# Kernel tuning notes

Measured on AMD Instinct MI355X. Metric: run time of the kernel, lower is better.

Reference implementation:

```python
import jax, jax.numpy as jnp
import numpy as np

B, S, D, H = 8, 1024, 512, 8
HD = D // H
EPS = 1e-5


def layer_norm(x, g, b):
    m = jnp.mean(x, axis=-1, keepdims=True)
    v = jnp.mean(jnp.square(x - m), axis=-1, keepdims=True)
    return (x - m) * jax.lax.rsqrt(v + EPS) * g + b


def mha(x, w_in, b_in, w_out, b_out):
    # x: [B,S,D]; w_in: [3D,D]; PyTorch MultiheadAttention math (no dropout, eval)
    b, s, d = x.shape
    qkv = x @ w_in.T + b_in                      # [B,S,3D]
    q, k, v = jnp.split(qkv, 3, axis=-1)
    q = q.reshape(b, s, H, HD)
    k = k.reshape(b, s, H, HD)
    v = v.reshape(b, s, H, HD)
    scores = jnp.einsum('bqhd,bkhd->bhqk', q, k) / np.sqrt(HD)
    a = jax.nn.softmax(scores, axis=-1)
    o = jnp.einsum('bhqk,bkhd->bqhd', a, v).reshape(b, s, d)
    return o @ w_out.T + b_out


def interp_linear(y, out_size):
    # y: [B,S_in,D]; torch F.interpolate(mode='linear', align_corners=False)
    s_in = y.shape[1]
    scale = s_in / out_size
    src = (jnp.arange(out_size, dtype=jnp.float32) + 0.5) * scale - 0.5
    src = jnp.clip(src, 0.0, s_in - 1.0)
    i0 = jnp.floor(src).astype(jnp.int32)
    i1 = jnp.minimum(i0 + 1, s_in - 1)
    w = (src - i0.astype(jnp.float32))[None, :, None]
    return y[:, i0, :] * (1.0 - w) + y[:, i1, :] * w


def setup_inputs() -> dict:
    key = jax.random.key(0)
    ks = jax.random.split(key, 16)
    sd = 0.02
    return {
        'x': jax.random.normal(ks[0], (B, S, D), jnp.float32),
        'w_in1': jax.random.normal(ks[1], (3 * D, D), jnp.float32) * sd,
        'b_in1': jnp.zeros((3 * D,), jnp.float32),
        'w_out1': jax.random.normal(ks[2], (D, D), jnp.float32) * sd,
        'b_out1': jnp.zeros((D,), jnp.float32),
        'w_in2': jax.random.normal(ks[3], (3 * D, D), jnp.float32) * sd,
        'b_in2': jnp.zeros((3 * D,), jnp.float32),
        'w_out2': jax.random.normal(ks[4], (D, D), jnp.float32) * sd,
        'b_out2': jnp.zeros((D,), jnp.float32),
        'g1': jnp.ones((D,), jnp.float32), 'beta1': jnp.zeros((D,), jnp.float32),
        'g2': jnp.ones((D,), jnp.float32), 'beta2': jnp.zeros((D,), jnp.float32),
        'g3': jnp.ones((D,), jnp.float32), 'beta3': jnp.zeros((D,), jnp.float32),
        'w_ff1': jax.random.normal(ks[5], (4 * D, D), jnp.float32) * sd,
        'b_ff1': jnp.zeros((4 * D,), jnp.float32),
        'w_ff2': jax.random.normal(ks[6], (D, 4 * D), jnp.float32) * sd,
        'b_ff2': jnp.zeros((D,), jnp.float32),
    }


def reference(x, w_in1, b_in1, w_out1, b_out1, w_in2, b_in2, w_out2, b_out2,
              g1, beta1, g2, beta2, g3, beta3, w_ff1, b_ff1, w_ff2, b_ff2):
    a1 = mha(x, w_in1, b_in1, w_out1, b_out1)
    x = layer_norm(x + a1, g1, beta1)
    # avg_pool1d kernel=2 stride=2 ceil_mode (S even -> exact halving)
    pooled = x.reshape(B, S // 2, 2, D).mean(axis=2)
    a2 = mha(pooled, w_in2, b_in2, w_out2, b_out2)
    up = interp_linear(a2, S)
    x = layer_norm(x + up, g2, beta2)
    h = jax.nn.gelu(x @ w_ff1.T + b_ff1, approximate=False)
    ff = h @ w_ff2.T + b_ff2
    return layer_norm(x + ff, g3, beta3)
```

## Files before the change

kernel.cpp:

```cpp
#include <hip/hip_runtime.h>
#include <hip/hip_bf16.h>
#include <math.h>

typedef __hip_bfloat16 bf16;
typedef __attribute__((ext_vector_type(8))) short short8;
typedef __attribute__((ext_vector_type(4))) float f32x4;
typedef __attribute__((ext_vector_type(16))) float f32x16;

__device__ __forceinline__ float ldf(const float* p, size_t i) { return p[i]; }
__device__ __forceinline__ float ldf(const bf16*  p, size_t i) { return __bfloat162float(p[i]); }
__device__ __forceinline__ void  stf(float* p, size_t i, float v) { p[i] = v; }
__device__ __forceinline__ void  stf(bf16*  p, size_t i, float v) { p[i] = __float2bfloat16(v); }

__device__ __forceinline__ float ex2(float x) { return __builtin_amdgcn_exp2f(x); }

__device__ __forceinline__ void gl16(const void* gp, void* lp) {
    __builtin_amdgcn_global_load_lds(
        (const __attribute__((address_space(1))) void*)gp,
        (__attribute__((address_space(3))) void*)lp, 16, 0, 0);
}

__device__ __forceinline__ void pl32swap(unsigned &a, unsigned &b) {
    asm volatile("v_permlane32_swap_b32 %0, %1" : "+v"(a), "+v"(b));
}

__global__ __launch_bounds__(256) void cvt_kernel(
    const float* __restrict__ src, bf16* __restrict__ dst, int n)
{
    for (int i = blockIdx.x * 256 + threadIdx.x; i < n; i += gridDim.x * 256)
        dst[i] = __float2bfloat16(src[i]);
}

__global__ __launch_bounds__(256) void cvt_w(
    const float* __restrict__ s0, const float* __restrict__ s1,
    const float* __restrict__ s2, const float* __restrict__ s3,
    const float* __restrict__ s4, const float* __restrict__ s5,
    bf16* __restrict__ dst)
{
    int i = blockIdx.x * 256 + threadIdx.x;
    const float* s; int off;
    if      (i <  786432) { s = s0; off = 0; }
    else if (i < 1048576) { s = s1; off =  786432; }
    else if (i < 1835008) { s = s2; off = 1048576; }
    else if (i < 2097152) { s = s3; off = 1835008; }
    else if (i < 3145728) { s = s4; off = 2097152; }
    else                  { s = s5; off = 3145728; }
    dst[i] = __float2bfloat16(s[i - off]);
}

__global__ __launch_bounds__(256) void vtrans(
    const bf16* __restrict__ qkv, bf16* __restrict__ vt, int S)
{
    __shared__ bf16 t[64][72];
    const int tid = threadIdx.x;
    const int s0 = blockIdx.x * 64;
    const int bh = blockIdx.y;
    const int b = bh >> 3, h = bh & 7;
    const int rr = tid >> 3, c8 = (tid & 7) * 8;
    #pragma unroll
    for (int p = 0; p < 2; p++) {
        int row = p * 32 + rr;
        *(short8*)&t[row][c8] =
            *(const short8*)&qkv[(size_t)(b * S + s0 + row) * 1536 + 1024 + h * 64 + c8];
    }
    __syncthreads();
    #pragma unroll
    for (int p = 0; p < 2; p++) {
        int d = p * 32 + rr;
        union { bf16 v[8]; short8 s; } pk;
        #pragma unroll
        for (int j = 0; j < 8; j++) pk.v[j] = t[c8 + j][d];
        *(short8*)&vt[(size_t)(bh * 64 + d) * S + s0 + c8] = pk.s;
    }
}

template <int EPI>
__global__ __launch_bounds__(256) void gemm_rs(
    const bf16* __restrict__ A, const bf16* __restrict__ W,
    const float* __restrict__ bias, bf16* __restrict__ C,
    int M, int N, int K)
{
    __shared__ __align__(16) bf16 Asl[2][128 * 64];
    __shared__ __align__(16) bf16 Bsl[2][128 * 64];

    const int tid  = threadIdx.x;
    const int lane = tid & 63;
    const int wave = tid >> 6;
    const int wm   = wave >> 1, wn = wave & 1;
    const int l15  = lane & 15, quad = lane >> 4;

    const int nwg = gridDim.x * gridDim.y;
    const int bid = blockIdx.y * gridDim.x + blockIdx.x;
    const int wid = (bid & 7) * (nwg >> 3) + (bid >> 3);
    const int bx  = wid % gridDim.x, by = wid / gridDim.x;
    const int row0 = by * 128, col0 = bx * 128;

    const int sr = tid >> 3;
    const int gg = tid & 7;

    const bf16* As[4]; const bf16* Ws[4]; int lo[4];
    #pragma unroll
    for (int j = 0; j < 4; j++) {
        int row = j * 32 + sr;
        int gs  = (gg ^ (row & 7)) * 8;
        As[j] = &A[(size_t)(row0 + row) * K + gs];
        Ws[j] = &W[(size_t)(col0 + row) * K + gs];
        lo[j] = row * 64 + gg * 8;
    }

    short8 ga[4], gb[4];
    auto LOADG = [&](int k0) {
        #pragma unroll
        for (int j = 0; j < 4; j++) ga[j] = *(const short8*)(As[j] + k0);
        #pragma unroll
        for (int j = 0; j < 4; j++) gb[j] = *(const short8*)(Ws[j] + k0);
    };
    auto WRITEL = [&](int buf) {
        #pragma unroll
        for (int j = 0; j < 4; j++) {
            *(short8*)&Asl[buf][lo[j]] = ga[j];
            *(short8*)&Bsl[buf][lo[j]] = gb[j];
        }
    };

    f32x4 acc[4][4] = {};
    const int nk = K >> 6;

    LOADG(0);
    WRITEL(0);
    __syncthreads();

    int cur = 0;
    for (int i = 0; i < nk; i++) {
        if (i + 1 < nk) LOADG((i + 1) << 6);

        #pragma unroll
        for (int ks = 0; ks < 64; ks += 32) {
            short8 af[4], bfr[4];
            const int g0 = (ks >> 3) + quad;
            const int col = (g0 ^ (l15 & 7)) * 8;
            #pragma unroll
            for (int mt = 0; mt < 4; mt++)
                af[mt] = *(const short8*)&Asl[cur][(wm * 64 + mt * 16 + l15) * 64 + col];
            #pragma unroll
            for (int nt = 0; nt < 4; nt++)
                bfr[nt] = *(const short8*)&Bsl[cur][(wn * 64 + nt * 16 + l15) * 64 + col];
            #pragma unroll
            for (int mt = 0; mt < 4; mt++)
                #pragma unroll
                for (int nt = 0; nt < 4; nt++)
                    acc[mt][nt] = __builtin_amdgcn_mfma_f32_16x16x32_bf16(
                        af[mt], bfr[nt], acc[mt][nt], 0, 0, 0);
        }

        if (i + 1 < nk) WRITEL(cur ^ 1);
        __syncthreads();
        cur ^= 1;
    }

    #pragma unroll
    for (int mt = 0; mt < 4; mt++) {
        int row = row0 + wm * 64 + mt * 16 + quad * 4;
        #pragma unroll
        for (int nt = 0; nt < 4; nt++) {
            int col = col0 + wn * 64 + nt * 16 + l15;
            float bv = bias[col];
            #pragma unroll
            for (int r = 0; r < 4; r++) {
                float v = acc[mt][nt][r] + bv;
                if (EPI == 1) v = 0.5f * v * (1.0f + erff(v * 0.70710678118654752f));
                C[(size_t)(row + r) * N + col] = __float2bfloat16(v);
            }
        }
    }
}

template <int LQB>
__global__ __launch_bounds__(128) void flash_attn_mfma(
    const bf16* __restrict__ qkv, const bf16* __restrict__ vt,
    bf16* __restrict__ o)
{
    constexpr int S  = 64 << LQB;
    constexpr int nt = 1 << LQB;

    __shared__ __align__(16) bf16 Kl[2][64 * 64];

    const int tid  = threadIdx.x;
    const int wave = tid >> 6, lane = tid & 63;
    const int l31  = lane & 31, hi = lane >> 5;

    const int r    = blockIdx.x;
    const int w    = (r & 7) * ((1 << LQB) * 8) + (r >> 3);
    const int qblk = w & ((1 << LQB) - 1);
    const int bh   = w >> LQB;
    const int h    = bh & 7, bb = bh >> 3;
    const int q0   = qblk * 64 + wave * 32;

    const bf16* base  = qkv + (size_t)bb * S * 1536 + h * 64;
    const bf16* vbase = vt + (size_t)bh * 64 * S;

    short8 qf[4];
    #pragma unroll
    for (int c = 0; c < 4; c++)
        qf[c] = *(const short8*)&base[(size_t)(q0 + l31) * 1536 + c * 16 + hi * 8];

    const int sr = lane >> 3;
    const int sc = ((lane & 7) ^ sr) * 8;

    auto STGK = [&](int buf, int k0) {
        #pragma unroll
        for (int t = 0; t < 4; t++) {
            int r0 = wave * 32 + t * 8;
            gl16(&base[(size_t)(k0 + r0 + sr) * 1536 + 512 + sc], &Kl[buf][r0 * 64]);
        }
    };

    f32x16 oacc[2] = {};
    float lrow = 0.f;
    const float CE = 0.18033688f;

    STGK(0, 0);

    for (int it = 0; it < nt; it++) {
        const int cur = it & 1;
        __syncthreads();
        if (it + 1 < nt) STGK(cur ^ 1, (it + 1) << 6);

        short8 vf[2][2][2];
        {
            const bf16* vb = vbase + (it << 6) + hi * 8;
            #pragma unroll
            for (int dt = 0; dt < 2; dt++) {
                const bf16* vd = &vb[(size_t)(dt * 32 + l31) * S];
                #pragma unroll
                for (int sub = 0; sub < 2; sub++)
                    #pragma unroll
                    for (int kk = 0; kk < 2; kk++)
                        vf[sub][kk][dt] = *(const short8*)&vd[sub * 32 + kk * 16];
            }
        }

        const bf16* Kc = &Kl[cur][0];
        #pragma unroll
        for (int sub = 0; sub < 2; sub++) {
            f32x16 st = {};
            #pragma unroll
            for (int c = 0; c < 4; c++) {
                const int row  = sub * 32 + l31;
                const int slot = (c * 2 + hi) ^ (row & 7);
                short8 af = *(const short8*)&Kc[row * 64 + slot * 8];
                st = __builtin_amdgcn_mfma_f32_32x32x16_bf16(af, qf[c], st, 0, 0, 0);
            }

            float p[16]; float ps = 0.f;
            #pragma unroll
            for (int r2 = 0; r2 < 16; r2++) {
                p[r2] = ex2(st[r2] * CE - 2.0f);
                ps += p[r2];
            }
            lrow += ps;

            unsigned wk[8];
            #pragma unroll
            for (int j = 0; j < 8; j++)
                asm("v_cvt_pk_bf16_f32 %0, %1, %2" : "=v"(wk[j]) : "v"(p[2*j]), "v"(p[2*j+1]));

            #pragma unroll
            for (int kk = 0; kk < 2; kk++) {
                pl32swap(wk[kk*4+0], wk[kk*4+2]);
                pl32swap(wk[kk*4+1], wk[kk*4+3]);
                union { unsigned u[4]; short8 s; } pa;
                pa.u[0] = wk[kk*4+0]; pa.u[1] = wk[kk*4+1];
                pa.u[2] = wk[kk*4+2]; pa.u[3] = wk[kk*4+3];
                #pragma unroll
                for (int dt = 0; dt < 2; dt++)
                    oacc[dt] = __builtin_amdgcn_mfma_f32_32x32x16_bf16(
                        pa.s, vf[sub][kk][dt], oacc[dt], 0, 0, 0);
            }
        }
    }

    lrow += __shfl_xor(lrow, 32);
    float inv = 1.0f / lrow;
    #pragma unroll
    for (int r2 = 0; r2 < 16; r2++) {
        int qr = (r2 & 3) + 8 * (r2 >> 2) + 4 * hi;
        float iv = __shfl(inv, qr);
        size_t rb = ((size_t)bb * S + q0 + qr) * 512 + h * 64;
        o[rb + l31]      = __float2bfloat16(oacc[0][r2] * iv);
        o[rb + 32 + l31] = __float2bfloat16(oacc[1][r2] * iv);
    }
}

template <typename AT, typename OT, bool INTERP>
__global__ __launch_bounds__(256) void ln_kernel(
    const AT* __restrict__ a, const bf16* __restrict__ bsrc,
    const float* __restrict__ g, const float* __restrict__ beta,
    OT* __restrict__ out)
{
    const int row = blockIdx.x;
    const int t = threadIdx.x;
    const size_t base = (size_t)row * 512;

    float a0 = ldf(a, base + t), a1 = ldf(a, base + t + 256);
    float b0, b1;
    if (INTERP) {
        int s = row & 1023, bb = row >> 10;
        float src = fminf(fmaxf((s + 0.5f) * 0.5f - 0.5f, 0.f), 511.f);
        int i0 = (int)src;
        int i1 = min(i0 + 1, 511);
        float w = src - (float)i0;
        size_t r0 = ((size_t)bb * 512 + i0) * 512;
        size_t r1 = ((size_t)bb * 512 + i1) * 512;
        b0 = __bfloat162float(bsrc[r0 + t]) * (1.f - w) + __bfloat162float(bsrc[r1 + t]) * w;
        b1 = __bfloat162float(bsrc[r0 + t + 256]) * (1.f - w) + __bfloat162float(bsrc[r1 + t + 256]) * w;
    } else {
        b0 = __bfloat162float(bsrc[base + t]);
        b1 = __bfloat162float(bsrc[base + t + 256]);
    }
    float v0 = a0 + b0, v1 = a1 + b1;

    __shared__ float red[4];
    const int lane = t & 63, wid = t >> 6;

    float sm = v0 + v1;
    #pragma unroll
    for (int off = 32; off > 0; off >>= 1) sm += __shfl_xor(sm, off);
    if (lane == 0) red[wid] = sm;
    __syncthreads();
    sm = red[0] + red[1] + red[2] + red[3];
    const float mean = sm * (1.0f / 512.0f);

    float d0 = v0 - mean, d1 = v1 - mean;
    float vv = d0 * d0 + d1 * d1;
    __syncthreads();
    #pragma unroll
    for (int off = 32; off > 0; off >>= 1) vv += __shfl_xor(vv, off);
    if (lane == 0) red[wid] = vv;
    __syncthreads();
    vv = red[0] + red[1] + red[2] + red[3];
    const float rstd = rsqrtf(vv * (1.0f / 512.0f) + 1e-5f);

    stf(out, base + t,       d0 * rstd * g[t]       + beta[t]);
    stf(out, base + t + 256, d1 * rstd * g[t + 256] + beta[t + 256]);
}

__global__ __launch_bounds__(256) void pool_kernel(
    const bf16* __restrict__ x, bf16* __restrict__ p)
{
    size_t i = (size_t)blockIdx.x * 256 + threadIdx.x;
    size_t d = i & 511;
    size_t rs = i >> 9;
    size_t b = rs >> 9, s = rs & 511;
    size_t r = (b * 1024 + 2 * s) * 512 + d;
    p[i] = __float2bfloat16(0.5f * (__bfloat162float(x[r]) + __bfloat162float(x[r + 512])));
}

extern "C" void kernel_launch(void* const* d_in, const int* in_sizes, int n_in,
                              void* d_out, int out_size, void* d_ws, size_t ws_size,
                              hipStream_t stream)
{
    const float* x      = (const float*)d_in[0];
    const float* w_in1  = (const float*)d_in[1];
    const float* b_in1  = (const float*)d_in[2];
    const float* w_out1 = (const float*)d_in[3];
    const float* b_out1 = (const float*)d_in[4];
    const float* w_in2  = (const float*)d_in[5];
    const float* b_in2  = (const float*)d_in[6];
    const float* w_out2 = (const float*)d_in[7];
    const float* b_out2 = (const float*)d_in[8];
    const float* g1     = (const float*)d_in[9];
    const float* be1    = (const float*)d_in[10];
    const float* g2     = (const float*)d_in[11];
    const float* be2    = (const float*)d_in[12];
    const float* g3     = (const float*)d_in[13];
    const float* be3    = (const float*)d_in[14];
    const float* w_ff1  = (const float*)d_in[15];
    const float* b_ff1  = (const float*)d_in[16];
    const float* w_ff2  = (const float*)d_in[17];
    const float* b_ff2  = (const float*)d_in[18];

    bf16* ws     = (bf16*)d_ws;
    bf16* xb     = ws + 0;
    bf16* wq1    = ws + 4194304;
    bf16* wo1    = ws + 4980736;
    bf16* wq2    = ws + 5242880;
    bf16* wo2    = ws + 6029312;
    bf16* wf1    = ws + 6291456;
    bf16* wf2    = ws + 7340032;
    bf16* qkv1   = ws + 8388608;
    bf16* o1     = ws + 20971520;
    bf16* a1     = ws + 25165824;
    bf16* x1     = ws + 29360128;
    bf16* pooled = ws + 33554432;
    bf16* qkv2   = ws + 35651584;
    bf16* o2     = ws + 41943040;
    bf16* a2     = ws + 44040192;
    bf16* x2     = ws + 46137344;
    bf16* h      = ws + 8388608;
    bf16* ff     = ws + 25165824;
    bf16* vt     = ws + 46137344;

    dim3 blk(256);
    dim3 fblk(128);

    cvt_kernel<<<4096, blk, 0, stream>>>(x, xb, 4194304);
    cvt_w<<<16384, blk, 0, stream>>>(w_in1, w_out1, w_in2, w_out2, w_ff1, w_ff2, wq1);

    gemm_rs<0><<<dim3(12, 64), blk, 0, stream>>>(xb, wq1, b_in1, qkv1, 8192, 1536, 512);
    vtrans<<<dim3(16, 64), blk, 0, stream>>>(qkv1, vt, 1024);
    flash_attn_mfma<4><<<dim3(1024), fblk, 0, stream>>>(qkv1, vt, o1);
    gemm_rs<0><<<dim3(4, 64), blk, 0, stream>>>(o1, wo1, b_out1, a1, 8192, 512, 512);
    ln_kernel<float, bf16, false><<<8192, blk, 0, stream>>>(x, a1, g1, be1, x1);
    pool_kernel<<<8192, blk, 0, stream>>>(x1, pooled);
    gemm_rs<0><<<dim3(12, 32), blk, 0, stream>>>(pooled, wq2, b_in2, qkv2, 4096, 1536, 512);
    vtrans<<<dim3(8, 64), blk, 0, stream>>>(qkv2, vt, 512);
    flash_attn_mfma<3><<<dim3(512), fblk, 0, stream>>>(qkv2, vt, o2);
    gemm_rs<0><<<dim3(4, 32), blk, 0, stream>>>(o2, wo2, b_out2, a2, 4096, 512, 512);
    ln_kernel<bf16, bf16, true><<<8192, blk, 0, stream>>>(x1, a2, g2, be2, x2);
    gemm_rs<1><<<dim3(16, 64), blk, 0, stream>>>(x2, wf1, b_ff1, h, 8192, 2048, 512);
    gemm_rs<0><<<dim3(4, 64), blk, 0, stream>>>(h, wf2, b_ff2, ff, 8192, 512, 2048);
    ln_kernel<bf16, float, false><<<8192, blk, 0, stream>>>(x2, ff, g3, be3, (float*)d_out);
}
```

Baseline: 322.4 us.

## Fuse V transpose into QKV GEMM epilogue, fuse LN with pooling, narrow N tiles

The QKV projection GEMM now writes the V columns straight into the transposed vt layout in its epilogue, so the separate vtrans kernels go away. The first layernorm and the average pool are merged into one kernel that handles row pairs and writes both x1 and pooled. The GEMM gains a BN template parameter, and the N=512 GEMMs and the second QKV GEMM use 64-wide tiles to launch more workgroups. Together these cut kernel launches and the extra reads of qkv and x1. The costs are narrower 8-byte scattered stores in the vt epilogue and lower per-tile data reuse in the narrow GEMMs.

```diff
diff --git a/kernel.cpp b/kernel.cpp
--- a/kernel.cpp
+++ b/kernel.cpp
@@ -48,40 +48,18 @@
     dst[i] = __float2bfloat16(s[i - off]);
 }
 
-__global__ __launch_bounds__(256) void vtrans(
-    const bf16* __restrict__ qkv, bf16* __restrict__ vt, int S)
-{
-    __shared__ bf16 t[64][72];
-    const int tid = threadIdx.x;
-    const int s0 = blockIdx.x * 64;
-    const int bh = blockIdx.y;
-    const int b = bh >> 3, h = bh & 7;
-    const int rr = tid >> 3, c8 = (tid & 7) * 8;
-    #pragma unroll
-    for (int p = 0; p < 2; p++) {
-        int row = p * 32 + rr;
-        *(short8*)&t[row][c8] =
-            *(const short8*)&qkv[(size_t)(b * S + s0 + row) * 1536 + 1024 + h * 64 + c8];
-    }
-    __syncthreads();
-    #pragma unroll
-    for (int p = 0; p < 2; p++) {
-        int d = p * 32 + rr;
-        union { bf16 v[8]; short8 s; } pk;
-        #pragma unroll
-        for (int j = 0; j < 8; j++) pk.v[j] = t[c8 + j][d];
-        *(short8*)&vt[(size_t)(bh * 64 + d) * S + s0 + c8] = pk.s;
-    }
-}
-
-template <int EPI>
+template <int EPI, int BN, int VS>
 __global__ __launch_bounds__(256) void gemm_rs(
     const bf16* __restrict__ A, const bf16* __restrict__ W,
     const float* __restrict__ bias, bf16* __restrict__ C,
-    int M, int N, int K)
-{
+    bf16* __restrict__ vt, int M, int N, int K)
+{
+    constexpr int WNC = BN / 2;
+    constexpr int NT  = BN / 32;
+    constexpr int RB  = BN / 32;
+
     __shared__ __align__(16) bf16 Asl[2][128 * 64];
-    __shared__ __align__(16) bf16 Bsl[2][128 * 64];
+    __shared__ __align__(16) bf16 Bsl[2][BN * 64];
 
     const int tid  = threadIdx.x;
     const int lane = tid & 63;
@@ -93,37 +71,42 @@
     const int bid = blockIdx.y * gridDim.x + blockIdx.x;
     const int wid = (bid & 7) * (nwg >> 3) + (bid >> 3);
     const int bx  = wid % gridDim.x, by = wid / gridDim.x;
-    const int row0 = by * 128, col0 = bx * 128;
+    const int row0 = by * 128, col0 = bx * BN;
 
     const int sr = tid >> 3;
     const int gg = tid & 7;
 
-    const bf16* As[4]; const bf16* Ws[4]; int lo[4];
+    const bf16* As[4]; const bf16* Ws[RB]; int loA[4], loB[RB];
     #pragma unroll
     for (int j = 0; j < 4; j++) {
         int row = j * 32 + sr;
         int gs  = (gg ^ (row & 7)) * 8;
-        As[j] = &A[(size_t)(row0 + row) * K + gs];
-        Ws[j] = &W[(size_t)(col0 + row) * K + gs];
-        lo[j] = row * 64 + gg * 8;
-    }
-
-    short8 ga[4], gb[4];
+        As[j]  = &A[(size_t)(row0 + row) * K + gs];
+        loA[j] = row * 64 + gg * 8;
+    }
+    #pragma unroll
+    for (int j = 0; j < RB; j++) {
+        int row = j * 32 + sr;
+        int gs  = (gg ^ (row & 7)) * 8;
+        Ws[j]  = &W[(size_t)(col0 + row) * K + gs];
+        loB[j] = row * 64 + gg * 8;
+    }
+
+    short8 ga[4], gb[RB];
     auto LOADG = [&](int k0) {
         #pragma unroll
         for (int j = 0; j < 4; j++) ga[j] = *(const short8*)(As[j] + k0);
         #pragma unroll
-        for (int j = 0; j < 4; j++) gb[j] = *(const short8*)(Ws[j] + k0);
+        for (int j = 0; j < RB; j++) gb[j] = *(const short8*)(Ws[j] + k0);
     };
     auto WRITEL = [&](int buf) {
         #pragma unroll
-        for (int j = 0; j < 4; j++) {
-            *(short8*)&Asl[buf][lo[j]] = ga[j];
-            *(short8*)&Bsl[buf][lo[j]] = gb[j];
-        }
+        for (int j = 0; j < 4; j++) *(short8*)&Asl[buf][loA[j]] = ga[j];
+        #pragma unroll
+        for (int j = 0; j < RB; j++) *(short8*)&Bsl[buf][loB[j]] = gb[j];
     };
 
-    f32x4 acc[4][4] = {};
+    f32x4 acc[4][NT] = {};
     const int nk = K >> 6;
 
     LOADG(0);
@@ -136,19 +119,19 @@
 
         #pragma unroll
         for (int ks = 0; ks < 64; ks += 32) {
-            short8 af[4], bfr[4];
+            short8 af[4], bfr[NT];
             const int g0 = (ks >> 3) + quad;
             const int col = (g0 ^ (l15 & 7)) * 8;
             #pragma unroll
             for (int mt = 0; mt < 4; mt++)
                 af[mt] = *(const short8*)&Asl[cur][(wm * 64 + mt * 16 + l15) * 64 + col];
             #pragma unroll
-            for (int nt = 0; nt < 4; nt++)
-                bfr[nt] = *(const short8*)&Bsl[cur][(wn * 64 + nt * 16 + l15) * 64 + col];
+            for (int nt = 0; nt < NT; nt++)
+                bfr[nt] = *(const short8*)&Bsl[cur][(wn * WNC + nt * 16 + l15) * 64 + col];
             #pragma unroll
             for (int mt = 0; mt < 4; mt++)
                 #pragma unroll
-                for (int nt = 0; nt < 4; nt++)
+                for (int nt = 0; nt < NT; nt++)
                     acc[mt][nt] = __builtin_amdgcn_mfma_f32_16x16x32_bf16(
                         af[mt], bfr[nt], acc[mt][nt], 0, 0, 0);
         }
@@ -158,12 +141,37 @@
         cur ^= 1;
     }
 
+    if constexpr (VS > 0) {
+        if (col0 >= 1024) {
+            constexpr int LS = (VS == 1024) ? 10 : 9;
+            #pragma unroll
+            for (int mt = 0; mt < 4; mt++) {
+                int rowm = row0 + wm * 64 + mt * 16 + quad * 4;
+                int b8 = rowm >> LS;
+                int s4 = rowm & (VS - 1);
+                #pragma unroll
+                for (int nt = 0; nt < NT; nt++) {
+                    int col = col0 + wn * WNC + nt * 16 + l15;
+                    float bv = bias[col];
+                    int hd = col - 1024;
+                    union { bf16 b4[4]; unsigned long long u; } pk;
+                    #pragma unroll
+                    for (int r = 0; r < 4; r++)
+                        pk.b4[r] = __float2bfloat16(acc[mt][nt][r] + bv);
+                    *(unsigned long long*)&vt[
+                        ((size_t)(b8 * 8 + (hd >> 6)) * 64 + (hd & 63)) * VS + s4] = pk.u;
+                }
+            }
+            return;
+        }
+    }
+
     #pragma unroll
     for (int mt = 0; mt < 4; mt++) {
         int row = row0 + wm * 64 + mt * 16 + quad * 4;
         #pragma unroll
-        for (int nt = 0; nt < 4; nt++) {
-            int col = col0 + wn * 64 + nt * 16 + l15;
+        for (int nt = 0; nt < NT; nt++) {
+            int col = col0 + wn * WNC + nt * 16 + l15;
             float bv = bias[col];
             #pragma unroll
             for (int r = 0; r < 4; r++) {
@@ -345,15 +353,62 @@
     stf(out, base + t + 256, d1 * rstd * g[t + 256] + beta[t + 256]);
 }
 
-__global__ __launch_bounds__(256) void pool_kernel(
-    const bf16* __restrict__ x, bf16* __restrict__ p)
-{
-    size_t i = (size_t)blockIdx.x * 256 + threadIdx.x;
-    size_t d = i & 511;
-    size_t rs = i >> 9;
-    size_t b = rs >> 9, s = rs & 511;
-    size_t r = (b * 1024 + 2 * s) * 512 + d;
-    p[i] = __float2bfloat16(0.5f * (__bfloat162float(x[r]) + __bfloat162float(x[r + 512])));
+__global__ __launch_bounds__(256) void ln_pool_kernel(
+    const float* __restrict__ a, const bf16* __restrict__ bsrc,
+    const float* __restrict__ g, const float* __restrict__ beta,
+    bf16* __restrict__ x1, bf16* __restrict__ pooled)
+{
+    const int pr = blockIdx.x;
+    const int t = threadIdx.x;
+    const size_t base0 = (size_t)(2 * pr) * 512;
+    const size_t base1 = base0 + 512;
+
+    float u0 = a[base0 + t]       + __bfloat162float(bsrc[base0 + t]);
+    float u1 = a[base0 + t + 256] + __bfloat162float(bsrc[base0 + t + 256]);
+    float w0 = a[base1 + t]       + __bfloat162float(bsrc[base1 + t]);
+    float w1 = a[base1 + t + 256] + __bfloat162float(bsrc[base1 + t + 256]);
+
+    __shared__ float red[2][4];
+    const int lane = t & 63, wid = t >> 6;
+
+    float s0 = u0 + u1, s1 = w0 + w1;
+    #pragma unroll
+    for (int off = 32; off > 0; off >>= 1) {
+        s0 += __shfl_xor(s0, off);
+        s1 += __shfl_xor(s1, off);
+    }
+    if (lane == 0) { red[0][wid] = s0; red[1][wid] = s1; }
+    __syncthreads();
+    const float m0 = (red[0][0] + red[0][1] + red[0][2] + red[0][3]) * (1.0f / 512.0f);
+    const float m1 = (red[1][0] + red[1][1] + red[1][2] + red[1][3]) * (1.0f / 512.0f);
+
+    float du0 = u0 - m0, du1 = u1 - m0, dw0 = w0 - m1, dw1 = w1 - m1;
+    float v0 = du0 * du0 + du1 * du1, v1 = dw0 * dw0 + dw1 * dw1;
+    __syncthreads();
+    #pragma unroll
+    for (int off = 32; off > 0; off >>= 1) {
+        v0 += __shfl_xor(v0, off);
+        v1 += __shfl_xor(v1, off);
+    }
+    if (lane == 0) { red[0][wid] = v0; red[1][wid] = v1; }
+    __syncthreads();
+    const float r0 = rsqrtf((red[0][0] + red[0][1] + red[0][2] + red[0][3]) * (1.0f / 512.0f) + 1e-5f);
+    const float r1 = rsqrtf((red[1][0] + red[1][1] + red[1][2] + red[1][3]) * (1.0f / 512.0f) + 1e-5f);
+
+    float g0 = g[t], g1v = g[t + 256], be0 = beta[t], be1 = beta[t + 256];
+    float y00 = du0 * r0 * g0  + be0;
+    float y01 = du1 * r0 * g1v + be1;
+    float y10 = dw0 * r1 * g0  + be0;
+    float y11 = dw1 * r1 * g1v + be1;
+
+    x1[base0 + t]       = __float2bfloat16(y00);
+    x1[base0 + t + 256] = __float2bfloat16(y01);
+    x1[base1 + t]       = __float2bfloat16(y10);
+    x1[base1 + t + 256] = __float2bfloat16(y11);
+
+    const size_t pb = (size_t)pr * 512;
+    pooled[pb + t]       = __float2bfloat16(0.5f * (y00 + y10));
+    pooled[pb + t + 256] = __float2bfloat16(0.5f * (y01 + y11));
 }
 
 extern "C" void kernel_launch(void* const* d_in, const int* in_sizes, int n_in,
@@ -407,18 +462,15 @@
     cvt_kernel<<<4096, blk, 0, stream>>>(x, xb, 4194304);
     cvt_w<<<16384, blk, 0, stream>>>(w_in1, w_out1, w_in2, w_out2, w_ff1, w_ff2, wq1);
 
-    gemm_rs<0><<<dim3(12, 64), blk, 0, stream>>>(xb, wq1, b_in1, qkv1, 8192, 1536, 512);
-    vtrans<<<dim3(16, 64), blk, 0, stream>>>(qkv1, vt, 1024);
+    gemm_rs<0,128,1024><<<dim3(12, 64), blk, 0, stream>>>(xb, wq1, b_in1, qkv1, vt, 8192, 1536, 512);
     flash_attn_mfma<4><<<dim3(1024), fblk, 0, stream>>>(qkv1, vt, o1);
-    gemm_rs<0><<<dim3(4, 64), blk, 0, stream>>>(o1, wo1, b_out1, a1, 8192, 512, 512);
-    ln_kernel<float, bf16, false><<<8192, blk, 0, stream>>>(x, a1, g1, be1, x1);
-    pool_kernel<<<8192, blk, 0, stream>>>(x1, pooled);
-    gemm_rs<0><<<dim3(12, 32), blk, 0, stream>>>(pooled, wq2, b_in2, qkv2, 4096, 1536, 512);
-    vtrans<<<dim3(8, 64), blk, 0, stream>>>(qkv2, vt, 512);
+    gemm_rs<0,64,0><<<dim3(8, 64), blk, 0, stream>>>(o1, wo1, b_out1, a1, nullptr, 8192, 512, 512);
+    ln_pool_kernel<<<4096, blk, 0, stream>>>(x, a1, g1, be1, x1, pooled);
+    gemm_rs<0,64,512><<<dim3(24, 32), blk, 0, stream>>>(pooled, wq2, b_in2, qkv2, vt, 4096, 1536, 512);
     flash_attn_mfma<3><<<dim3(512), fblk, 0, stream>>>(qkv2, vt, o2);
-    gemm_rs<0><<<dim3(4, 32), blk, 0, stream>>>(o2, wo2, b_out2, a2, 4096, 512, 512);
+    gemm_rs<0,64,0><<<dim3(8, 32), blk, 0, stream>>>(o2, wo2, b_out2, a2, nullptr, 4096, 512, 512);
     ln_kernel<bf16, bf16, true><<<8192, blk, 0, stream>>>(x1, a2, g2, be2, x2);
-    gemm_rs<1><<<dim3(16, 64), blk, 0, stream>>>(x2, wf1, b_ff1, h, 8192, 2048, 512);
-    gemm_rs<0><<<dim3(4, 64), blk, 0, stream>>>(h, wf2, b_ff2, ff, 8192, 512, 2048);
+    gemm_rs<1,128,0><<<dim3(16, 64), blk, 0, stream>>>(x2, wf1, b_ff1, h, nullptr, 8192, 2048, 512);
+    gemm_rs<0,64,0><<<dim3(8, 64), blk, 0, stream>>>(h, wf2, b_ff2, ff, nullptr, 8192, 512, 2048);
     ln_kernel<bf16, float, false><<<8192, blk, 0, stream>>>(x2, ff, g3, be3, (float*)d_out);
 }
```

New measurement: 311.7 us. 1.03x faster.
